# Optimization experiments

Measured on AMD Instinct MI355X. Metric: run time of the kernel, lower is better.

## Reference

```python
import jax, jax.numpy as jnp
import numpy as np

DIM = 768

def setup_inputs() -> dict:
    key = jax.random.key(0)
    ks = jax.random.split(key, 11)
    B, N = 4, 2048
    s = 1.0 / np.sqrt(DIM)
    inp = {
        "q": jax.random.normal(ks[0], (B, N, DIM), jnp.float32),
        "k": jax.random.normal(ks[1], (B, N, DIM), jnp.float32),
        "v": jax.random.normal(ks[2], (B, N, DIM), jnp.float32),
        "Wq": jax.random.normal(ks[3], (DIM, DIM), jnp.float32) * s,
        "bq": jnp.zeros((DIM,), jnp.float32),
        "Wk": jax.random.normal(ks[4], (DIM, DIM), jnp.float32) * s,
        "bk": jnp.zeros((DIM,), jnp.float32),
        "Wv": jax.random.normal(ks[5], (DIM, DIM), jnp.float32) * s,
        "bv": jnp.zeros((DIM,), jnp.float32),
        "Wp": jax.random.normal(ks[6], (DIM, DIM), jnp.float32) * s,
        "bp": jnp.zeros((DIM,), jnp.float32),
    }
    return inp

def reference(q, k, v, Wq, bq, Wk, bk, Wv, bv, Wp, bp):
    # Linear projections (torch Linear: x @ W.T + b)
    scale = DIM ** (-0.5)  # note: full dim, num_heads unused in original forward
    qp = q @ Wq.T + bq            # [B, Nq, D]
    kp = k @ Wk.T + bk            # [B, Nk, D]
    vp = v @ Wv.T + bv            # [B, Nk, D]
    attn = jnp.einsum('bqd,bkd->bqk', qp * scale, kp)  # [B, Nq, Nk]
    attn = jax.nn.softmax(attn, axis=-1)
    x = jnp.einsum('bqk,bkd->bqd', attn, vp)           # [B, Nq, D]
    return x @ Wp.T + bp
```

## Files before the change

### kernel.cpp

```cpp
#include <hip/hip_runtime.h>
#include <hip/hip_bf16.h>
#include <math.h>

typedef __bf16 bf16x8 __attribute__((ext_vector_type(8)));
typedef float  f32x4  __attribute__((ext_vector_type(4)));
typedef float  f32x4v __attribute__((ext_vector_type(4)));
typedef unsigned short ushort_t;
typedef ushort_t u16x4 __attribute__((ext_vector_type(4)));
typedef ushort_t u16x8 __attribute__((ext_vector_type(8)));

__device__ __forceinline__ ushort_t f2bf(float f) {
    unsigned u = __builtin_bit_cast(unsigned, f);
    u += 0x7FFFu + ((u >> 16) & 1u);
    return (ushort_t)(u >> 16);
}
__device__ __forceinline__ float bf2f(ushort_t b) {
    return __builtin_bit_cast(float, (unsigned)b << 16);
}

__device__ __forceinline__ void xcd_remap(int& bx, int& by, int& bz) {
    const int gx = gridDim.x, gy = gridDim.y;
    const int nwg = gx * gy * gridDim.z;
    const int lin = (blockIdx.z * gy + blockIdx.y) * gx + blockIdx.x;
    const int chunk = nwg >> 3;
    int nid = (lin & 7) * chunk + (lin >> 3);
    bx = nid % gx; nid /= gx;
    by = nid % gy; bz = nid / gy;
}

__global__ __launch_bounds__(256) void cvt_multi(const float* __restrict__ i0, const float* __restrict__ i1,
                                                 const float* __restrict__ i2, const float* __restrict__ i3,
                                                 ushort_t* __restrict__ o0, ushort_t* __restrict__ o1,
                                                 ushort_t* __restrict__ o2, ushort_t* __restrict__ o3, int n4) {
    const int z = blockIdx.z;
    const float* in  = z == 0 ? i0 : z == 1 ? i1 : z == 2 ? i2 : i3;
    ushort_t*    out = z == 0 ? o0 : z == 1 ? o1 : z == 2 ? o2 : o3;
    int i = blockIdx.x * 256 + threadIdx.x;
    if (i >= n4) return;
    f32x4v v = ((const f32x4v*)in)[i];
    u16x4 o = { f2bf(v.x), f2bf(v.y), f2bf(v.z), f2bf(v.w) };
    ((u16x4*)out)[i] = o;
}

__global__ __launch_bounds__(256) void zero_f32(float* __restrict__ p, int n) {
    int i = blockIdx.x * 256 + threadIdx.x;
    if (i < n) p[i] = 0.f;
}

#define GEMM256_CORE(Ab_, lda_, Bb_, ldb_, Kdim_)                                           \
    __shared__ __align__(16) ushort_t lds[2][2][2][128 * 64];                               \
    const int tid  = threadIdx.x;                                                           \
    const int lane = tid & 63;                                                              \
    const int wave = tid >> 6;                                                              \
    const int wm = wave >> 2, wn = wave & 3;                                                \
    const int r16 = lane & 15, kb = lane >> 4;                                              \
    f32x4 acc[8][4];                                                                        \
    _Pragma("unroll") for (int i = 0; i < 8; ++i)                                           \
        _Pragma("unroll") for (int j = 0; j < 4; ++j)                                       \
            acc[i][j] = (f32x4){0.f, 0.f, 0.f, 0.f};                                        \
    auto stage = [&](int kt) {                                                              \
        const int d  = kt & 1;                                                              \
        const int k0 = kt * 64;                                                             \
        _Pragma("unroll") for (int arr = 0; arr < 2; ++arr)                                 \
        _Pragma("unroll") for (int h = 0; h < 2; ++h)                                       \
        _Pragma("unroll") for (int l = 0; l < 2; ++l) {                                     \
            const int idx = l * 512 + tid;                                                  \
            const int row = idx >> 3, sl = idx & 7;                                         \
            const int ssrc = sl ^ (row & 7);                                                \
            const long long grow = h * 128 + row;                                           \
            const ushort_t* g = (arr == 0)                                                  \
                ? (Ab_) + (tM + grow) * (long long)(lda_) + k0 + ssrc * 8                   \
                : (Bb_) + (tN + grow) * (long long)(ldb_) + k0 + ssrc * 8;                  \
            ushort_t* lp = &lds[d][arr][h][idx * 8];                                        \
            __builtin_amdgcn_global_load_lds((const __attribute__((address_space(1))) void*)g, \
                                             (__attribute__((address_space(3))) void*)lp, 16, 0, 0); \
        }                                                                                   \
    };                                                                                      \
    auto compute = [&](int kt) {                                                            \
        const int d = kt & 1;                                                               \
        _Pragma("unroll") for (int kk = 0; kk < 2; ++kk) {                                  \
            bf16x8 bfr[4];                                                                  \
            _Pragma("unroll") for (int ni = 0; ni < 4; ++ni) {                              \
                const int row = (wn & 1) * 64 + ni * 16 + r16;                              \
                const int o16 = row * 8 + ((kk * 4 + kb) ^ (row & 7));                      \
                bfr[ni] = *(const bf16x8*)((const char*)&lds[d][1][wn >> 1][0] + o16 * 16); \
            }                                                                               \
            __builtin_amdgcn_s_setprio(1);                                                  \
            _Pragma("unroll") for (int mi = 0; mi < 8; ++mi) {                              \
                const int row = mi * 16 + r16;                                              \
                const int o16 = row * 8 + ((kk * 4 + kb) ^ (row & 7));                      \
                bf16x8 af = *(const bf16x8*)((const char*)&lds[d][0][wm][0] + o16 * 16);    \
                _Pragma("unroll") for (int ni = 0; ni < 4; ++ni)                            \
                    acc[mi][ni] = __builtin_amdgcn_mfma_f32_16x16x32_bf16(af, bfr[ni], acc[mi][ni], 0, 0, 0); \
            }                                                                               \
            __builtin_amdgcn_s_setprio(0);                                                  \
        }                                                                                   \
    };                                                                                      \
    const int NT = (Kdim_) / 64;                                                            \
    stage(0);                                                                               \
    __syncthreads();                                                                        \
    for (int t = 0; t < NT; ++t) {                                                          \
        if (t + 1 < NT) stage(t + 1);                                                       \
        compute(t);                                                                         \
        __syncthreads();                                                                    \
    }                                                                                       \
    const int rquad = (lane >> 4) * 4;                                                      \
    const int cl    = lane & 15;

__global__ __launch_bounds__(512, 2)
void sexp256(const ushort_t* __restrict__ qp, const ushort_t* __restrict__ kp,
             ushort_t* __restrict__ P, float* __restrict__ rowsum, float scale)
{
    int bx, by, bz;
    xcd_remap(bx, by, bz);
    const long long tM = (long long)by * 256;
    const long long tN = (long long)bx * 256;
    const int z = bz;
    const ushort_t* Ab = qp + (long long)z * 1572864;
    const ushort_t* Bb = kp + (long long)z * 1572864;

    GEMM256_CORE(Ab, 768, Bb, 768, 768)

    ushort_t* out = P + (long long)z * 4194304;
#pragma unroll
    for (int mi = 0; mi < 8; ++mi) {
        const long long r = tM + wm * 128 + mi * 16 + rquad;
        float rs[4] = {0.f, 0.f, 0.f, 0.f};
#pragma unroll
        for (int ni = 0; ni < 4; ++ni) {
            f32x4 v = acc[mi][ni];
            const long long c = tN + wn * 64 + ni * 16 + cl;
#pragma unroll
            for (int j = 0; j < 4; ++j) {
                float p = __expf(v[j] * scale);
                ushort_t pb = f2bf(p);
                out[(r + j) * 2048 + c] = pb;
                rs[j] += bf2f(pb);
            }
        }
#pragma unroll
        for (int j = 0; j < 4; ++j) {
            float s = rs[j];
            s += __shfl_xor(s, 1, 64);
            s += __shfl_xor(s, 2, 64);
            s += __shfl_xor(s, 4, 64);
            s += __shfl_xor(s, 8, 64);
            if (cl == 0) atomicAdd(&rowsum[(long long)z * 2048 + r + j], s);
        }
    }
}

__global__ __launch_bounds__(512, 2)
void proj256(const ushort_t* __restrict__ a0, const ushort_t* __restrict__ a1, const ushort_t* __restrict__ a2,
             const ushort_t* __restrict__ w0, const ushort_t* __restrict__ w1, const ushort_t* __restrict__ w2,
             const float* __restrict__ b0, const float* __restrict__ b1, const float* __restrict__ b2,
             ushort_t* __restrict__ dq, ushort_t* __restrict__ dk, ushort_t* __restrict__ dvT)
{
    int bx, by, bz;
    xcd_remap(bx, by, bz);
    const int z = bz;
    const long long tM = (z < 2) ? (long long)by * 256 : (long long)bx * 256;
    const long long tN = (z < 2) ? (long long)bx * 256 : (long long)by * 256;
    const ushort_t* Ab = z == 0 ? a0 : z == 1 ? a1 : w2;
    const ushort_t* Bb = z == 0 ? w0 : z == 1 ? w1 : a2;
    const float* bias  = z == 0 ? b0 : z == 1 ? b1 : b2;

    GEMM256_CORE(Ab, 768, Bb, 768, 768)

#pragma unroll
    for (int mi = 0; mi < 8; ++mi) {
        const long long r = tM + wm * 128 + mi * 16 + rquad;
        if (z < 2) {
            ushort_t* dst = z == 0 ? dq : dk;
#pragma unroll
            for (int ni = 0; ni < 4; ++ni) {
                f32x4 v = acc[mi][ni];
                const long long c = tN + wn * 64 + ni * 16 + cl;
                const float bc = bias[c];
#pragma unroll
                for (int j = 0; j < 4; ++j)
                    dst[(r + j) * 768 + c] = f2bf(v[j] + bc);
            }
        } else {
#pragma unroll
            for (int ni = 0; ni < 4; ++ni) {
                f32x4 v = acc[mi][ni];
                const long long c = tN + wn * 64 + ni * 16 + cl;
#pragma unroll
                for (int j = 0; j < 4; ++j)
                    dvT[(r + j) * 8192 + c] = f2bf(v[j] + bias[r + j]);
            }
        }
    }
}

#define M_PVN  1
#define M_OUT  2

#define BM 128
#define BN 128
#define BK 32

#define GEMM_CORE(Ab_, lda_, Bb_, ldb_, Kdim_)                                              \
    __shared__ __align__(16) ushort_t lds[2][2][BM * BK];                                   \
    const int tid  = threadIdx.x;                                                           \
    const int lane = tid & 63;                                                              \
    const int wave = tid >> 6;                                                              \
    const int wr = wave >> 1, wc = wave & 1;                                                \
    f32x4 acc[4][4];                                                                        \
    _Pragma("unroll") for (int i = 0; i < 4; ++i)                                           \
        _Pragma("unroll") for (int j = 0; j < 4; ++j)                                       \
            acc[i][j] = (f32x4){0.f, 0.f, 0.f, 0.f};                                        \
    auto stage = [&](int buf, int kt) {                                                     \
        const int k0 = kt * BK;                                                             \
        _Pragma("unroll") for (int rnd = 0; rnd < 2; ++rnd) {                               \
            const int c    = tid + rnd * 256;                                               \
            const int row  = c >> 2;                                                        \
            const int slot = (c & 3) ^ (row & 3);                                           \
            const ushort_t* ga = (Ab_) + (tM + row) * (long long)(lda_) + k0 + slot * 8;    \
            const ushort_t* gb = (Bb_) + (tN + row) * (long long)(ldb_) + k0 + slot * 8;    \
            ushort_t* la = &lds[buf][0][(rnd * 256 + wave * 64) * 8];                       \
            ushort_t* lb = &lds[buf][1][(rnd * 256 + wave * 64) * 8];                       \
            __builtin_amdgcn_global_load_lds((const __attribute__((address_space(1))) void*)ga, \
                                             (__attribute__((address_space(3))) void*)la, 16, 0, 0); \
            __builtin_amdgcn_global_load_lds((const __attribute__((address_space(1))) void*)gb, \
                                             (__attribute__((address_space(3))) void*)lb, 16, 0, 0); \
        }                                                                                   \
    };                                                                                      \
    auto compute = [&](int buf) {                                                           \
        const int kb  = lane >> 4;                                                          \
        const int r16 = lane & 15;                                                          \
        bf16x8 af[4], bfr[4];                                                               \
        _Pragma("unroll") for (int mi = 0; mi < 4; ++mi) {                                  \
            const int row = wr * 64 + mi * 16 + r16;                                        \
            const int off = row * 64 + ((kb ^ (row & 3)) << 4);                             \
            af[mi] = *(const bf16x8*)((const char*)lds[buf][0] + off);                      \
        }                                                                                   \
        _Pragma("unroll") for (int ni = 0; ni < 4; ++ni) {                                  \
            const int row = wc * 64 + ni * 16 + r16;                                        \
            const int off = row * 64 + ((kb ^ (row & 3)) << 4);                             \
            bfr[ni] = *(const bf16x8*)((const char*)lds[buf][1] + off);                     \
        }                                                                                   \
        _Pragma("unroll") for (int mi = 0; mi < 4; ++mi)                                    \
            _Pragma("unroll") for (int ni = 0; ni < 4; ++ni)                                \
                acc[mi][ni] = __builtin_amdgcn_mfma_f32_16x16x32_bf16(af[mi], bfr[ni], acc[mi][ni], 0, 0, 0); \
    };                                                                                      \
    const int NT = (Kdim_) / BK;                                                            \
    stage(0, 0);                                                                            \
    __syncthreads();                                                                        \
    int cur = 0;                                                                            \
    for (int kt = 0; kt + 1 < NT; ++kt) {                                                   \
        stage(cur ^ 1, kt + 1);                                                             \
        compute(cur);                                                                       \
        __syncthreads();                                                                    \
        cur ^= 1;                                                                           \
    }                                                                                       \
    compute(cur);                                                                           \
    const int rquad = (lane >> 4) * 4;                                                      \
    const int cl    = lane & 15;

template<int MODE>
__global__ __launch_bounds__(256, 3)
void gemm_nt(const ushort_t* __restrict__ A, int lda, long long aBatch,
             const ushort_t* __restrict__ B, int ldb, long long bBatch,
             void* __restrict__ Cv, int ldc, long long cBatch,
             const float* __restrict__ bias, float* __restrict__ rowsum,
             int K)
{
    int bx, by, bz;
    xcd_remap(bx, by, bz);
    const long long tM = (long long)by * BM;
    const long long tN = (long long)bx * BN;
    const int z = bz;
    const ushort_t* Ab = A + (long long)z * aBatch;
    const ushort_t* Bb = B + (long long)z * bBatch;

    GEMM_CORE(Ab, lda, Bb, ldb, K)

#pragma unroll
    for (int mi = 0; mi < 4; ++mi) {
        const long long r = tM + wr * 64 + mi * 16 + rquad;
        if constexpr (MODE == M_PVN) {
            ushort_t* out = (ushort_t*)Cv + (long long)z * cBatch;
            float inv[4];
#pragma unroll
            for (int j = 0; j < 4; ++j)
                inv[j] = 1.0f / rowsum[(long long)z * 2048 + r + j];
#pragma unroll
            for (int ni = 0; ni < 4; ++ni) {
                f32x4 v = acc[mi][ni];
                const long long c = tN + wc * 64 + ni * 16 + cl;
#pragma unroll
                for (int j = 0; j < 4; ++j)
                    out[(r + j) * ldc + c] = f2bf(v[j] * inv[j]);
            }
        } else {
            float* out = (float*)Cv;
#pragma unroll
            for (int ni = 0; ni < 4; ++ni) {
                f32x4 v = acc[mi][ni];
                const long long c = tN + wc * 64 + ni * 16 + cl;
                const float bc = bias[c];
#pragma unroll
                for (int j = 0; j < 4; ++j)
                    out[(r + j) * ldc + c] = v[j] + bc;
            }
        }
    }
}

extern "C" void kernel_launch(void* const* d_in, const int* in_sizes, int n_in,
                              void* d_out, int out_size, void* d_ws, size_t ws_size,
                              hipStream_t stream) {
    (void)in_sizes; (void)n_in; (void)out_size; (void)ws_size;
    const float* q  = (const float*)d_in[0];
    const float* k  = (const float*)d_in[1];
    const float* v  = (const float*)d_in[2];
    const float* Wq = (const float*)d_in[3];
    const float* bq = (const float*)d_in[4];
    const float* Wk = (const float*)d_in[5];
    const float* bk = (const float*)d_in[6];
    const float* Wv = (const float*)d_in[7];
    const float* bv = (const float*)d_in[8];
    const float* Wp = (const float*)d_in[9];
    const float* bp = (const float*)d_in[10];
    float* out = (float*)d_out;

    char* ws = (char*)d_ws;
    ushort_t* qb  = (ushort_t*)(ws);
    ushort_t* kb  = (ushort_t*)(ws + 12582912LL);
    ushort_t* vb  = (ushort_t*)(ws + 25165824LL);
    ushort_t* P   = (ushort_t*)(ws);
    float* rowsum = (float*)(ws + 33554432LL);
    ushort_t* Wqb = (ushort_t*)(ws + 67108864LL);
    ushort_t* Wkb = (ushort_t*)(ws + 68288512LL);
    ushort_t* Wvb = (ushort_t*)(ws + 69468160LL);
    ushort_t* Wpb = (ushort_t*)(ws + 70647808LL);
    ushort_t* qp  = (ushort_t*)(ws + 71827456LL);
    ushort_t* kp  = (ushort_t*)(ws + 84410368LL);
    ushort_t* vpT = (ushort_t*)(ws + 96993280LL);
    ushort_t* Ob  = qp;

    const float scale = 1.0f / sqrtf(768.0f);

    cvt_multi<<<dim3(6144, 1, 3), 256, 0, stream>>>(q, k, v, nullptr, qb, kb, vb, nullptr, 1572864);
    cvt_multi<<<dim3(576, 1, 4), 256, 0, stream>>>(Wq, Wk, Wv, Wp, Wqb, Wkb, Wvb, Wpb, 147456);

    proj256<<<dim3(3, 32, 3), 512, 0, stream>>>(qb, kb, vb, Wqb, Wkb, Wvb, bq, bk, bv, qp, kp, vpT);

    zero_f32<<<32, 256, 0, stream>>>(rowsum, 8192);

    sexp256<<<dim3(8, 8, 4), 512, 0, stream>>>(qp, kp, P, rowsum, scale);

    gemm_nt<M_PVN><<<dim3(6, 16, 4), 256, 0, stream>>>(P, 2048, 4194304, vpT, 8192, 2048,
                                                       Ob, 768, 1572864, nullptr, rowsum, 2048);

    gemm_nt<M_OUT><<<dim3(6, 64, 1), 256, 0, stream>>>(Ob, 768, 0, Wpb, 768, 0, out, 768, 0, bp, nullptr, 768);
}
```

Before: 169.2 us.

## Split 256-tile GEMM into eight-phase pipeline and fuse V projection into score kernel

The 256x256 GEMM core now stages each half-tile separately and interleaves LDS reads, global-to-LDS loads and MFMA blocks across eight barrier-delimited phases per two K-steps, with explicit vmcnt waits. This is meant to hide load latency better than the single-stage double buffer. The V projection moves out of the projection launch and runs as extra workgroups inside the QK^T/exp kernel, so the Q/K projection grid shrinks and both grids are filled more evenly. The workspace is rearranged so P no longer overlaps vb, which the fused kernel still reads. The hand-written waitcnt and barrier schedule depends on exact load counts and could be fragile.

```diff
diff --git a/kernel.cpp b/kernel.cpp
--- a/kernel.cpp
+++ b/kernel.cpp
@@ -47,7 +47,27 @@
     if (i < n) p[i] = 0.f;
 }
 
-#define GEMM256_CORE(Ab_, lda_, Bb_, ldb_, Kdim_)                                           \
+#define S_BARR asm volatile("s_barrier" ::: "memory")
+
+#define PHASE8(tt_, q_, RDB_, STC_, STKT_, STARR_, STH_, VMW_)                              \
+    { bf16x8 af[2][2];                                                                      \
+      if (RDB_) rd_B((tt_), bfr);                                                           \
+      rd_Aq((tt_), (q_), af);                                                               \
+      if (STC_) stage_h((STKT_), (STARR_), (STH_));                                         \
+      S_BARR;                                                                               \
+      asm volatile("s_waitcnt lgkmcnt(0)" ::: "memory");                                    \
+      __builtin_amdgcn_sched_barrier(0);                                                    \
+      __builtin_amdgcn_s_setprio(1);                                                        \
+      _Pragma("unroll") for (int m2 = 0; m2 < 2; ++m2)                                      \
+      _Pragma("unroll") for (int ni = 0; ni < 4; ++ni)                                      \
+      _Pragma("unroll") for (int kk = 0; kk < 2; ++kk)                                      \
+          acc[(q_)*2 + m2][ni] = __builtin_amdgcn_mfma_f32_16x16x32_bf16(                   \
+              af[m2][kk], bfr[ni][kk], acc[(q_)*2 + m2][ni], 0, 0, 0);                      \
+      __builtin_amdgcn_s_setprio(0);                                                        \
+      VMW_;                                                                                 \
+      S_BARR; }
+
+#define GEMM256_8PH(Ab_, lda_, Bb_, ldb_, Kdim_)                                            \
     __shared__ __align__(16) ushort_t lds[2][2][2][128 * 64];                               \
     const int tid  = threadIdx.x;                                                           \
     const int lane = tid & 63;                                                              \
@@ -55,14 +75,12 @@
     const int wm = wave >> 2, wn = wave & 3;                                                \
     const int r16 = lane & 15, kb = lane >> 4;                                              \
     f32x4 acc[8][4];                                                                        \
-    _Pragma("unroll") for (int i = 0; i < 8; ++i)                                           \
-        _Pragma("unroll") for (int j = 0; j < 4; ++j)                                       \
-            acc[i][j] = (f32x4){0.f, 0.f, 0.f, 0.f};                                        \
-    auto stage = [&](int kt) {                                                              \
+    _Pragma("unroll") for (int i_ = 0; i_ < 8; ++i_)                                        \
+        _Pragma("unroll") for (int j_ = 0; j_ < 4; ++j_)                                    \
+            acc[i_][j_] = (f32x4){0.f, 0.f, 0.f, 0.f};                                      \
+    auto stage_h = [&](int kt, int arr, int h) {                                            \
         const int d  = kt & 1;                                                              \
         const int k0 = kt * 64;                                                             \
-        _Pragma("unroll") for (int arr = 0; arr < 2; ++arr)                                 \
-        _Pragma("unroll") for (int h = 0; h < 2; ++h)                                       \
         _Pragma("unroll") for (int l = 0; l < 2; ++l) {                                     \
             const int idx = l * 512 + tid;                                                  \
             const int row = idx >> 3, sl = idx & 7;                                         \
@@ -71,124 +89,154 @@
             const ushort_t* g = (arr == 0)                                                  \
                 ? (Ab_) + (tM + grow) * (long long)(lda_) + k0 + ssrc * 8                   \
                 : (Bb_) + (tN + grow) * (long long)(ldb_) + k0 + ssrc * 8;                  \
-            ushort_t* lp = &lds[d][arr][h][idx * 8];                                        \
             __builtin_amdgcn_global_load_lds((const __attribute__((address_space(1))) void*)g, \
-                                             (__attribute__((address_space(3))) void*)lp, 16, 0, 0); \
-        }                                                                                   \
-    };                                                                                      \
-    auto compute = [&](int kt) {                                                            \
+                (__attribute__((address_space(3))) void*)&lds[d][arr][h][idx * 8], 16, 0, 0); \
+        } };                                                                                \
+    auto rd_B = [&](int kt, bf16x8 (&bfr_)[4][2]) {                                         \
         const int d = kt & 1;                                                               \
+        _Pragma("unroll") for (int ni = 0; ni < 4; ++ni)                                    \
         _Pragma("unroll") for (int kk = 0; kk < 2; ++kk) {                                  \
-            bf16x8 bfr[4];                                                                  \
-            _Pragma("unroll") for (int ni = 0; ni < 4; ++ni) {                              \
-                const int row = (wn & 1) * 64 + ni * 16 + r16;                              \
-                const int o16 = row * 8 + ((kk * 4 + kb) ^ (row & 7));                      \
-                bfr[ni] = *(const bf16x8*)((const char*)&lds[d][1][wn >> 1][0] + o16 * 16); \
-            }                                                                               \
-            __builtin_amdgcn_s_setprio(1);                                                  \
-            _Pragma("unroll") for (int mi = 0; mi < 8; ++mi) {                              \
-                const int row = mi * 16 + r16;                                              \
-                const int o16 = row * 8 + ((kk * 4 + kb) ^ (row & 7));                      \
-                bf16x8 af = *(const bf16x8*)((const char*)&lds[d][0][wm][0] + o16 * 16);    \
-                _Pragma("unroll") for (int ni = 0; ni < 4; ++ni)                            \
-                    acc[mi][ni] = __builtin_amdgcn_mfma_f32_16x16x32_bf16(af, bfr[ni], acc[mi][ni], 0, 0, 0); \
-            }                                                                               \
-            __builtin_amdgcn_s_setprio(0);                                                  \
-        }                                                                                   \
-    };                                                                                      \
+            const int row = (wn & 1) * 64 + ni * 16 + r16;                                  \
+            const int o16 = row * 8 + ((kk * 4 + kb) ^ (row & 7));                          \
+            bfr_[ni][kk] = *(const bf16x8*)((const char*)&lds[d][1][wn >> 1][0] + o16 * 16);\
+        } };                                                                                \
+    auto rd_Aq = [&](int kt, int q, bf16x8 (&af_)[2][2]) {                                  \
+        const int d = kt & 1;                                                               \
+        _Pragma("unroll") for (int m2 = 0; m2 < 2; ++m2)                                    \
+        _Pragma("unroll") for (int kk = 0; kk < 2; ++kk) {                                  \
+            const int row = (q * 2 + m2) * 16 + r16;                                        \
+            const int o16 = row * 8 + ((kk * 4 + kb) ^ (row & 7));                          \
+            af_[m2][kk] = *(const bf16x8*)((const char*)&lds[d][0][wm][0] + o16 * 16);      \
+        } };                                                                                \
     const int NT = (Kdim_) / 64;                                                            \
-    stage(0);                                                                               \
-    __syncthreads();                                                                        \
-    for (int t = 0; t < NT; ++t) {                                                          \
-        if (t + 1 < NT) stage(t + 1);                                                       \
-        compute(t);                                                                         \
-        __syncthreads();                                                                    \
+                          \
+    stage_h(0, 1, 0); stage_h(0, 1, 1);                                                     \
+    stage_h(0, 0, 0); stage_h(0, 0, 1);                                                     \
+    stage_h(1, 1, 0); stage_h(1, 1, 1);                                                     \
+    asm volatile("s_waitcnt vmcnt(4)" ::: "memory");                                        \
+    S_BARR;                                                                                 \
+    _Pragma("unroll 1") for (int it = 0; it < NT / 2; ++it) {                               \
+        const int t = 2 * it;                                                               \
+        const bool more = (t + 2 < NT);                                                     \
+        bf16x8 bfr[4][2];                                                                   \
+        PHASE8(t,     0, true,  true, t + 1, 0, 0, )                                        \
+        PHASE8(t,     1, false, true, t + 1, 0, 1, )                                        \
+        PHASE8(t,     2, false, more, t + 2, 1, 0, )                                        \
+        PHASE8(t,     3, false, more, t + 2, 1, 1,                                          \
+               if (more) asm volatile("s_waitcnt vmcnt(4)" ::: "memory");                   \
+               else      asm volatile("s_waitcnt vmcnt(0)" ::: "memory"))                   \
+        PHASE8(t + 1, 0, true,  more, t + 2, 0, 0, )                                        \
+        PHASE8(t + 1, 1, false, more, t + 2, 0, 1, )                                        \
+        PHASE8(t + 1, 2, false, more, t + 3, 1, 0, )                                        \
+        PHASE8(t + 1, 3, false, more, t + 3, 1, 1,                                          \
+               if (more) asm volatile("s_waitcnt vmcnt(4)" ::: "memory"))                   \
     }                                                                                       \
     const int rquad = (lane >> 4) * 4;                                                      \
     const int cl    = lane & 15;
 
 __global__ __launch_bounds__(512, 2)
-void sexp256(const ushort_t* __restrict__ qp, const ushort_t* __restrict__ kp,
-             ushort_t* __restrict__ P, float* __restrict__ rowsum, float scale)
-{
-    int bx, by, bz;
-    xcd_remap(bx, by, bz);
-    const long long tM = (long long)by * 256;
-    const long long tN = (long long)bx * 256;
-    const int z = bz;
-    const ushort_t* Ab = qp + (long long)z * 1572864;
-    const ushort_t* Bb = kp + (long long)z * 1572864;
-
-    GEMM256_CORE(Ab, 768, Bb, 768, 768)
-
-    ushort_t* out = P + (long long)z * 4194304;
-#pragma unroll
-    for (int mi = 0; mi < 8; ++mi) {
-        const long long r = tM + wm * 128 + mi * 16 + rquad;
-        float rs[4] = {0.f, 0.f, 0.f, 0.f};
-#pragma unroll
-        for (int ni = 0; ni < 4; ++ni) {
-            f32x4 v = acc[mi][ni];
-            const long long c = tN + wn * 64 + ni * 16 + cl;
-#pragma unroll
-            for (int j = 0; j < 4; ++j) {
-                float p = __expf(v[j] * scale);
-                ushort_t pb = f2bf(p);
-                out[(r + j) * 2048 + c] = pb;
-                rs[j] += bf2f(pb);
-            }
-        }
-#pragma unroll
-        for (int j = 0; j < 4; ++j) {
-            float s = rs[j];
-            s += __shfl_xor(s, 1, 64);
-            s += __shfl_xor(s, 2, 64);
-            s += __shfl_xor(s, 4, 64);
-            s += __shfl_xor(s, 8, 64);
-            if (cl == 0) atomicAdd(&rowsum[(long long)z * 2048 + r + j], s);
-        }
-    }
-}
-
-__global__ __launch_bounds__(512, 2)
-void proj256(const ushort_t* __restrict__ a0, const ushort_t* __restrict__ a1, const ushort_t* __restrict__ a2,
-             const ushort_t* __restrict__ w0, const ushort_t* __restrict__ w1, const ushort_t* __restrict__ w2,
-             const float* __restrict__ b0, const float* __restrict__ b1, const float* __restrict__ b2,
-             ushort_t* __restrict__ dq, ushort_t* __restrict__ dk, ushort_t* __restrict__ dvT)
+void projqk8(const ushort_t* __restrict__ qin, const ushort_t* __restrict__ kin,
+             const ushort_t* __restrict__ Wqb, const ushort_t* __restrict__ Wkb,
+             const float* __restrict__ bqv, const float* __restrict__ bkv,
+             ushort_t* __restrict__ dq, ushort_t* __restrict__ dk)
 {
     int bx, by, bz;
     xcd_remap(bx, by, bz);
     const int z = bz;
-    const long long tM = (z < 2) ? (long long)by * 256 : (long long)bx * 256;
-    const long long tN = (z < 2) ? (long long)bx * 256 : (long long)by * 256;
-    const ushort_t* Ab = z == 0 ? a0 : z == 1 ? a1 : w2;
-    const ushort_t* Bb = z == 0 ? w0 : z == 1 ? w1 : a2;
-    const float* bias  = z == 0 ? b0 : z == 1 ? b1 : b2;
-
-    GEMM256_CORE(Ab, 768, Bb, 768, 768)
+    const long long tM = (long long)by * 256;
+    const long long tN = (long long)bx * 256;
+    const ushort_t* Ab = z ? kin : qin;
+    const ushort_t* Bb = z ? Wkb : Wqb;
+    const float* bias  = z ? bkv : bqv;
+    ushort_t* dst      = z ? dk : dq;
+
+    GEMM256_8PH(Ab, 768, Bb, 768, 768)
 
 #pragma unroll
     for (int mi = 0; mi < 8; ++mi) {
         const long long r = tM + wm * 128 + mi * 16 + rquad;
-        if (z < 2) {
-            ushort_t* dst = z == 0 ? dq : dk;
+#pragma unroll
+        for (int ni = 0; ni < 4; ++ni) {
+            f32x4 v = acc[mi][ni];
+            const long long c = tN + wn * 64 + ni * 16 + cl;
+            const float bc = bias[c];
+#pragma unroll
+            for (int j = 0; j < 4; ++j)
+                dst[(r + j) * 768 + c] = f2bf(v[j] + bc);
+        }
+    }
+}
+
+__global__ __launch_bounds__(512, 2)
+void sexp_pv8(const ushort_t* __restrict__ qp, const ushort_t* __restrict__ kp,
+              const ushort_t* __restrict__ Wvb, const ushort_t* __restrict__ vin,
+              const float* __restrict__ bvv,
+              ushort_t* __restrict__ P, float* __restrict__ rowsum,
+              ushort_t* __restrict__ dvT, float scale)
+{
+    int bx, by, bz;
+    xcd_remap(bx, by, bz);
+    const int wid = bx;
+    const bool is_pv = wid >= 256;
+    long long tM, tN;
+    const ushort_t *Ab, *Bb;
+    int z = 0;
+    if (!is_pv) {
+        z = wid >> 6;
+        const int w2 = wid & 63;
+        tM = (long long)(w2 >> 3) * 256;
+        tN = (long long)(w2 & 7) * 256;
+        Ab = qp + (long long)z * 1572864;
+        Bb = kp + (long long)z * 1572864;
+    } else {
+        const int pv = wid - 256;
+        tM = (long long)(pv >> 5) * 256;
+        tN = (long long)(pv & 31) * 256;
+        Ab = Wvb;
+        Bb = vin;
+    }
+
+    GEMM256_8PH(Ab, 768, Bb, 768, 768)
+
+    if (!is_pv) {
+        ushort_t* out = P + (long long)z * 4194304;
+#pragma unroll
+        for (int mi = 0; mi < 8; ++mi) {
+            const long long r = tM + wm * 128 + mi * 16 + rquad;
+            float rs[4] = {0.f, 0.f, 0.f, 0.f};
 #pragma unroll
             for (int ni = 0; ni < 4; ++ni) {
                 f32x4 v = acc[mi][ni];
                 const long long c = tN + wn * 64 + ni * 16 + cl;
-                const float bc = bias[c];
-#pragma unroll
-                for (int j = 0; j < 4; ++j)
-                    dst[(r + j) * 768 + c] = f2bf(v[j] + bc);
+#pragma unroll
+                for (int j = 0; j < 4; ++j) {
+                    float p = __expf(v[j] * scale);
+                    ushort_t pb = f2bf(p);
+                    out[(r + j) * 2048 + c] = pb;
+                    rs[j] += bf2f(pb);
+                }
             }
-        } else {
+#pragma unroll
+            for (int j = 0; j < 4; ++j) {
+                float s = rs[j];
+                s += __shfl_xor(s, 1, 64);
+                s += __shfl_xor(s, 2, 64);
+                s += __shfl_xor(s, 4, 64);
+                s += __shfl_xor(s, 8, 64);
+                if (cl == 0) atomicAdd(&rowsum[(long long)z * 2048 + r + j], s);
+            }
+        }
+    } else {
+#pragma unroll
+        for (int mi = 0; mi < 8; ++mi) {
+            const long long r = tM + wm * 128 + mi * 16 + rquad;
 #pragma unroll
             for (int ni = 0; ni < 4; ++ni) {
                 f32x4 v = acc[mi][ni];
                 const long long c = tN + wn * 64 + ni * 16 + cl;
 #pragma unroll
                 for (int j = 0; j < 4; ++j)
-                    dvT[(r + j) * 8192 + c] = f2bf(v[j] + bias[r + j]);
+                    dvT[(r + j) * 8192 + c] = f2bf(v[j] + bvv[r + j]);
             }
         }
     }
@@ -327,18 +375,18 @@
     float* out = (float*)d_out;
 
     char* ws = (char*)d_ws;
-    ushort_t* qb  = (ushort_t*)(ws);
-    ushort_t* kb  = (ushort_t*)(ws + 12582912LL);
-    ushort_t* vb  = (ushort_t*)(ws + 25165824LL);
-    ushort_t* P   = (ushort_t*)(ws);
-    float* rowsum = (float*)(ws + 33554432LL);
-    ushort_t* Wqb = (ushort_t*)(ws + 67108864LL);
-    ushort_t* Wkb = (ushort_t*)(ws + 68288512LL);
-    ushort_t* Wvb = (ushort_t*)(ws + 69468160LL);
-    ushort_t* Wpb = (ushort_t*)(ws + 70647808LL);
-    ushort_t* qp  = (ushort_t*)(ws + 71827456LL);
-    ushort_t* kp  = (ushort_t*)(ws + 84410368LL);
-    ushort_t* vpT = (ushort_t*)(ws + 96993280LL);
+    ushort_t* vb  = (ushort_t*)(ws);
+    ushort_t* qb  = (ushort_t*)(ws + 12582912LL);
+    ushort_t* kb  = (ushort_t*)(ws + 25165824LL);
+    ushort_t* P   = (ushort_t*)(ws + 12582912LL);
+    ushort_t* Wqb = (ushort_t*)(ws + 46137344LL);
+    ushort_t* Wkb = (ushort_t*)(ws + 47316992LL);
+    ushort_t* Wvb = (ushort_t*)(ws + 48496640LL);
+    ushort_t* Wpb = (ushort_t*)(ws + 49676288LL);
+    ushort_t* qp  = (ushort_t*)(ws + 50855936LL);
+    ushort_t* kp  = (ushort_t*)(ws + 63438848LL);
+    ushort_t* vpT = (ushort_t*)(ws + 76021760LL);
+    float* rowsum = (float*)(ws + 88604672LL);
     ushort_t* Ob  = qp;
 
     const float scale = 1.0f / sqrtf(768.0f);
@@ -346,11 +394,11 @@
     cvt_multi<<<dim3(6144, 1, 3), 256, 0, stream>>>(q, k, v, nullptr, qb, kb, vb, nullptr, 1572864);
     cvt_multi<<<dim3(576, 1, 4), 256, 0, stream>>>(Wq, Wk, Wv, Wp, Wqb, Wkb, Wvb, Wpb, 147456);
 
-    proj256<<<dim3(3, 32, 3), 512, 0, stream>>>(qb, kb, vb, Wqb, Wkb, Wvb, bq, bk, bv, qp, kp, vpT);
+    projqk8<<<dim3(3, 32, 2), 512, 0, stream>>>(qb, kb, Wqb, Wkb, bq, bk, qp, kp);
 
     zero_f32<<<32, 256, 0, stream>>>(rowsum, 8192);
 
-    sexp256<<<dim3(8, 8, 4), 512, 0, stream>>>(qp, kp, P, rowsum, scale);
+    sexp_pv8<<<dim3(352, 1, 1), 512, 0, stream>>>(qp, kp, Wvb, vb, bv, P, rowsum, vpT, scale);
 
     gemm_nt<M_PVN><<<dim3(6, 16, 4), 256, 0, stream>>>(P, 2048, 4194304, vpT, 8192, 2048,
                                                        Ob, 768, 1572864, nullptr, rowsum, 2048);
```

Measured after the change: 168.3 us. About the same (-0.6%).

## Overlap q/k conversion with V projection and merge small prep kernels

Applied to the files above, without the earlier changes.

The separate weight/input conversion and rowsum zeroing kernels are merged into one launch that converts v and all weights and clears rowsum. A new kernel runs the V projection GEMM on 96 blocks while the remaining blocks convert q and k to bf16 concurrently. The Q/K projections then run as their own kernel. This cuts launch count and tries to hide the memory-bound q/k conversion behind V-projection compute, at the cost of an extra launch boundary between the V and Q/K projections and a fixed block split that may be unbalanced.

```diff
diff --git a/kernel.cpp b/kernel.cpp
--- a/kernel.cpp
+++ b/kernel.cpp
@@ -28,23 +28,33 @@
     by = nid % gy; bz = nid / gy;
 }
 
-__global__ __launch_bounds__(256) void cvt_multi(const float* __restrict__ i0, const float* __restrict__ i1,
-                                                 const float* __restrict__ i2, const float* __restrict__ i3,
-                                                 ushort_t* __restrict__ o0, ushort_t* __restrict__ o1,
-                                                 ushort_t* __restrict__ o2, ushort_t* __restrict__ o3, int n4) {
-    const int z = blockIdx.z;
-    const float* in  = z == 0 ? i0 : z == 1 ? i1 : z == 2 ? i2 : i3;
-    ushort_t*    out = z == 0 ? o0 : z == 1 ? o1 : z == 2 ? o2 : o3;
-    int i = blockIdx.x * 256 + threadIdx.x;
-    if (i >= n4) return;
-    f32x4v v = ((const f32x4v*)in)[i];
-    u16x4 o = { f2bf(v.x), f2bf(v.y), f2bf(v.z), f2bf(v.w) };
-    ((u16x4*)out)[i] = o;
-}
-
-__global__ __launch_bounds__(256) void zero_f32(float* __restrict__ p, int n) {
-    int i = blockIdx.x * 256 + threadIdx.x;
-    if (i < n) p[i] = 0.f;
+__global__ __launch_bounds__(256)
+void cvt_all(const float* __restrict__ v, const float* __restrict__ Wq,
+             const float* __restrict__ Wk, const float* __restrict__ Wv,
+             const float* __restrict__ Wp,
+             ushort_t* __restrict__ vb, ushort_t* __restrict__ Wqb,
+             ushort_t* __restrict__ Wkb, ushort_t* __restrict__ Wvb,
+             ushort_t* __restrict__ Wpb, float* __restrict__ rowsum)
+{
+    const int b = blockIdx.x;
+    if (b < 6144) {
+        int i = b * 256 + threadIdx.x;
+        f32x4v x = ((const f32x4v*)v)[i];
+        u16x4 o = { f2bf(x.x), f2bf(x.y), f2bf(x.z), f2bf(x.w) };
+        ((u16x4*)vb)[i] = o;
+    } else if (b < 8448) {
+        const int w = (b - 6144) / 576;
+        const int bb = (b - 6144) % 576;
+        const float* in  = w == 0 ? Wq : w == 1 ? Wk : w == 2 ? Wv : Wp;
+        ushort_t*    out = w == 0 ? Wqb : w == 1 ? Wkb : w == 2 ? Wvb : Wpb;
+        int i = bb * 256 + threadIdx.x;
+        f32x4v x = ((const f32x4v*)in)[i];
+        u16x4 o = { f2bf(x.x), f2bf(x.y), f2bf(x.z), f2bf(x.w) };
+        ((u16x4*)out)[i] = o;
+    } else {
+        int i = (b - 8448) * 256 + threadIdx.x;
+        rowsum[i] = 0.f;
+    }
 }
 
 #define GEMM256_CORE(Ab_, lda_, Bb_, ldb_, Kdim_)                                           \
@@ -108,8 +118,82 @@
     const int cl    = lane & 15;
 
 __global__ __launch_bounds__(512, 2)
-void sexp256(const ushort_t* __restrict__ qp, const ushort_t* __restrict__ kp,
-             ushort_t* __restrict__ P, float* __restrict__ rowsum, float scale)
+void vprojcvt(const ushort_t* __restrict__ wv_, const ushort_t* __restrict__ vb_,
+              const float* __restrict__ bv_, ushort_t* __restrict__ dvT_,
+              const float* __restrict__ qf_, const float* __restrict__ kf_,
+              ushort_t* __restrict__ qb_, ushort_t* __restrict__ kb_)
+{
+    if (blockIdx.x < 96) {
+        const int id = blockIdx.x;
+        const long long tM = (long long)(id % 3) * 256;
+        const long long tN = (long long)(id / 3) * 256;
+        const ushort_t* Ab = wv_;
+        const ushort_t* Bb = vb_;
+
+        GEMM256_CORE(Ab, 768, Bb, 768, 768)
+
+#pragma unroll
+        for (int mi = 0; mi < 8; ++mi) {
+            const long long r = tM + wm * 128 + mi * 16 + rquad;
+#pragma unroll
+            for (int ni = 0; ni < 4; ++ni) {
+                f32x4 v = acc[mi][ni];
+                const long long c = tN + wn * 64 + ni * 16 + cl;
+#pragma unroll
+                for (int j = 0; j < 4; ++j)
+                    dvT_[(r + j) * 8192 + c] = f2bf(v[j] + bv_[r + j]);
+            }
+        }
+    } else {
+        const long long stride = 160LL * 512;
+        for (long long i = (long long)(blockIdx.x - 96) * 512 + threadIdx.x;
+             i < 2LL * 1572864; i += stride) {
+            const float* src; ushort_t* dst; long long off;
+            if (i < 1572864) { src = qf_; dst = qb_; off = i; }
+            else             { src = kf_; dst = kb_; off = i - 1572864; }
+            f32x4v v4 = ((const f32x4v*)src)[off];
+            u16x4 o = { f2bf(v4.x), f2bf(v4.y), f2bf(v4.z), f2bf(v4.w) };
+            ((u16x4*)dst)[off] = o;
+        }
+    }
+}
+
+__global__ __launch_bounds__(512, 2)
+void projqk2(const ushort_t* __restrict__ qin, const ushort_t* __restrict__ kin,
+             const ushort_t* __restrict__ Wqb, const ushort_t* __restrict__ Wkb,
+             const float* __restrict__ bqv, const float* __restrict__ bkv,
+             ushort_t* __restrict__ dq, ushort_t* __restrict__ dk)
+{
+    int bx, by, bz;
+    xcd_remap(bx, by, bz);
+    const int z = bz;
+    const long long tM = (long long)by * 256;
+    const long long tN = (long long)bx * 256;
+    const ushort_t* Ab = z ? kin : qin;
+    const ushort_t* Bb = z ? Wkb : Wqb;
+    const float* bias  = z ? bkv : bqv;
+    ushort_t* dst      = z ? dk : dq;
+
+    GEMM256_CORE(Ab, 768, Bb, 768, 768)
+
+#pragma unroll
+    for (int mi = 0; mi < 8; ++mi) {
+        const long long r = tM + wm * 128 + mi * 16 + rquad;
+#pragma unroll
+        for (int ni = 0; ni < 4; ++ni) {
+            f32x4 v = acc[mi][ni];
+            const long long c = tN + wn * 64 + ni * 16 + cl;
+            const float bc = bias[c];
+#pragma unroll
+            for (int j = 0; j < 4; ++j)
+                dst[(r + j) * 768 + c] = f2bf(v[j] + bc);
+        }
+    }
+}
+
+__global__ __launch_bounds__(512, 2)
+void sexp2(const ushort_t* __restrict__ qp, const ushort_t* __restrict__ kp,
+           ushort_t* __restrict__ P, float* __restrict__ rowsum, float scale)
 {
     int bx, by, bz;
     xcd_remap(bx, by, bz);
@@ -146,50 +230,6 @@
             s += __shfl_xor(s, 4, 64);
             s += __shfl_xor(s, 8, 64);
             if (cl == 0) atomicAdd(&rowsum[(long long)z * 2048 + r + j], s);
-        }
-    }
-}
-
-__global__ __launch_bounds__(512, 2)
-void proj256(const ushort_t* __restrict__ a0, const ushort_t* __restrict__ a1, const ushort_t* __restrict__ a2,
-             const ushort_t* __restrict__ w0, const ushort_t* __restrict__ w1, const ushort_t* __restrict__ w2,
-             const float* __restrict__ b0, const float* __restrict__ b1, const float* __restrict__ b2,
-             ushort_t* __restrict__ dq, ushort_t* __restrict__ dk, ushort_t* __restrict__ dvT)
-{
-    int bx, by, bz;
-    xcd_remap(bx, by, bz);
-    const int z = bz;
-    const long long tM = (z < 2) ? (long long)by * 256 : (long long)bx * 256;
-    const long long tN = (z < 2) ? (long long)bx * 256 : (long long)by * 256;
-    const ushort_t* Ab = z == 0 ? a0 : z == 1 ? a1 : w2;
-    const ushort_t* Bb = z == 0 ? w0 : z == 1 ? w1 : a2;
-    const float* bias  = z == 0 ? b0 : z == 1 ? b1 : b2;
-
-    GEMM256_CORE(Ab, 768, Bb, 768, 768)
-
-#pragma unroll
-    for (int mi = 0; mi < 8; ++mi) {
-        const long long r = tM + wm * 128 + mi * 16 + rquad;
-        if (z < 2) {
-            ushort_t* dst = z == 0 ? dq : dk;
-#pragma unroll
-            for (int ni = 0; ni < 4; ++ni) {
-                f32x4 v = acc[mi][ni];
-                const long long c = tN + wn * 64 + ni * 16 + cl;
-                const float bc = bias[c];
-#pragma unroll
-                for (int j = 0; j < 4; ++j)
-                    dst[(r + j) * 768 + c] = f2bf(v[j] + bc);
-            }
-        } else {
-#pragma unroll
-            for (int ni = 0; ni < 4; ++ni) {
-                f32x4 v = acc[mi][ni];
-                const long long c = tN + wn * 64 + ni * 16 + cl;
-#pragma unroll
-                for (int j = 0; j < 4; ++j)
-                    dvT[(r + j) * 8192 + c] = f2bf(v[j] + bias[r + j]);
-            }
         }
     }
 }
@@ -327,33 +367,31 @@
     float* out = (float*)d_out;
 
     char* ws = (char*)d_ws;
-    ushort_t* qb  = (ushort_t*)(ws);
-    ushort_t* kb  = (ushort_t*)(ws + 12582912LL);
-    ushort_t* vb  = (ushort_t*)(ws + 25165824LL);
-    ushort_t* P   = (ushort_t*)(ws);
-    float* rowsum = (float*)(ws + 33554432LL);
-    ushort_t* Wqb = (ushort_t*)(ws + 67108864LL);
-    ushort_t* Wkb = (ushort_t*)(ws + 68288512LL);
-    ushort_t* Wvb = (ushort_t*)(ws + 69468160LL);
-    ushort_t* Wpb = (ushort_t*)(ws + 70647808LL);
-    ushort_t* qp  = (ushort_t*)(ws + 71827456LL);
-    ushort_t* kp  = (ushort_t*)(ws + 84410368LL);
-    ushort_t* vpT = (ushort_t*)(ws + 96993280LL);
+    ushort_t* vb  = (ushort_t*)(ws);
+    ushort_t* qb  = (ushort_t*)(ws + 12582912LL);
+    ushort_t* kb  = (ushort_t*)(ws + 25165824LL);
+    ushort_t* P   = (ushort_t*)(ws + 12582912LL);
+    ushort_t* Wqb = (ushort_t*)(ws + 46137344LL);
+    ushort_t* Wkb = (ushort_t*)(ws + 47316992LL);
+    ushort_t* Wvb = (ushort_t*)(ws + 48496640LL);
+    ushort_t* Wpb = (ushort_t*)(ws + 49676288LL);
+    ushort_t* qp  = (ushort_t*)(ws + 50855936LL);
+    ushort_t* kp  = (ushort_t*)(ws + 63438848LL);
+    ushort_t* vpT = (ushort_t*)(ws + 76021760LL);
+    float* rowsum = (float*)(ws + 88604672LL);
     ushort_t* Ob  = qp;
 
     const float scale = 1.0f / sqrtf(768.0f);
 
-    cvt_multi<<<dim3(6144, 1, 3), 256, 0, stream>>>(q, k, v, nullptr, qb, kb, vb, nullptr, 1572864);
-    cvt_multi<<<dim3(576, 1, 4), 256, 0, stream>>>(Wq, Wk, Wv, Wp, Wqb, Wkb, Wvb, Wpb, 147456);
-
-    proj256<<<dim3(3, 32, 3), 512, 0, stream>>>(qb, kb, vb, Wqb, Wkb, Wvb, bq, bk, bv, qp, kp, vpT);
-
-    zero_f32<<<32, 256, 0, stream>>>(rowsum, 8192);
-
-    sexp256<<<dim3(8, 8, 4), 512, 0, stream>>>(qp, kp, P, rowsum, scale);
+    cvt_all<<<8480, 256, 0, stream>>>(v, Wq, Wk, Wv, Wp, vb, Wqb, Wkb, Wvb, Wpb, rowsum);
+
+    vprojcvt<<<256, 512, 0, stream>>>(Wvb, vb, bv, vpT, q, k, qb, kb);
+
+    projqk2<<<dim3(3, 32, 2), 512, 0, stream>>>(qb, kb, Wqb, Wkb, bq, bk, qp, kp);
+
+    sexp2<<<dim3(8, 8, 4), 512, 0, stream>>>(qp, kp, P, rowsum, scale);
 
     gemm_nt<M_PVN><<<dim3(6, 16, 4), 256, 0, stream>>>(P, 2048, 4194304, vpT, 8192, 2048,
                                                        Ob, 768, 1572864, nullptr, rowsum, 2048);
-
     gemm_nt<M_OUT><<<dim3(6, 64, 1), 256, 0, stream>>>(Ob, 768, 0, Wpb, 768, 0, out, 768, 0, bp, nullptr, 768);
 }
```

New measurement: 157.4 us. -7.0%, faster.
